# Kernel optimization log

Hardware: AMD Instinct MI355X
Metric: run time of the kernel (lower is better)

The kernel has to match this reference:

```python
import jax, jax.numpy as jnp
import numpy as np

B, N, C, H, D, Kd, Ff, L = 4, 4096, 512, 8, 64, 256, 2048, 2
EPS = 1e-5


def _ln(x, g, b):
    m = x.mean(-1, keepdims=True)
    v = ((x - m) ** 2).mean(-1, keepdims=True)
    return (x - m) / jnp.sqrt(v + EPS) * g + b


def setup_inputs() -> dict:
    key = jax.random.key(0)
    ks = jax.random.split(key, 20)
    s = 0.02
    return {
        'x': jax.random.normal(ks[0], (B, N, C), jnp.float32),
        'Wq': jax.random.normal(ks[1], (L, H, D, C), jnp.float32) * s,
        'Wk': jax.random.normal(ks[2], (L, H, D, C), jnp.float32) * s,
        'Wv': jax.random.normal(ks[3], (L, H, D, C), jnp.float32) * s,
        'Wo': jax.random.normal(ks[4], (L, C, H * D), jnp.float32) * s,
        'bo': jnp.zeros((L, C), jnp.float32),
        'ln1_g': jnp.ones((L, C), jnp.float32),
        'ln1_b': jnp.zeros((L, C), jnp.float32),
        'W1': jax.random.normal(ks[5], (L, Ff, C), jnp.float32) * s,
        'b1': jnp.zeros((L, Ff), jnp.float32),
        'W2': jax.random.normal(ks[6], (L, C, Ff), jnp.float32) * s,
        'b2': jnp.zeros((L, C), jnp.float32),
        'ln2_g': jnp.ones((L, C), jnp.float32),
        'ln2_b': jnp.zeros((L, C), jnp.float32),
        'Ew': jax.random.normal(ks[7], (Kd, N), jnp.float32) * (1.0 / np.sqrt(N)),
        'Eb': jnp.zeros((Kd,), jnp.float32),
    }


def reference(x, Wq, Wk, Wv, Wo, bo, ln1_g, ln1_b, W1, b1, W2, b2, ln2_g, ln2_b, Ew, Eb):
    # Linformer, layerwise-shared E=F projection, causal=False, eval mode (dropout off).
    n_layers = Wq.shape[0]
    d = Wq.shape[2]
    scale = 1.0 / jnp.sqrt(jnp.asarray(d, x.dtype))
    for l in range(n_layers):
        # per-head projections, all heads at once: [b,h,n,d]
        Q = jnp.einsum('bnc,hdc->bhnd', x, Wq[l])
        K = jnp.einsum('bnc,hdc->bhnd', x, Wk[l])
        V = jnp.einsum('bnc,hdc->bhnd', x, Wv[l])
        # E projection along seq axis: K^T [b,h,d,n] -> [b,h,d,k]
        Kp = jnp.einsum('bhnd,kn->bhdk', K, Ew) + Eb[None, None, None, :]
        P = jax.nn.softmax(jnp.einsum('bhnd,bhdk->bhnk', Q, Kp) * scale, axis=-1)
        # F projection (= E, layerwise sharing): V^T -> [b,h,k,d]
        Vp = jnp.einsum('bhnd,kn->bhkd', V, Ew) + Eb[None, None, :, None]
        o = jnp.einsum('bhnk,bhkd->bhnd', P, Vp)
        b_, h_, n_, d_ = o.shape
        o = o.transpose(0, 2, 1, 3).reshape(b_, n_, h_ * d_)  # concat heads
        o = o @ Wo[l].T + bo[l]
        x = _ln(x + o, ln1_g[l], ln1_b[l])  # post-norm residual
        f = jax.nn.gelu(x @ W1[l].T + b1[l], approximate=False) @ W2[l].T + b2[l]
        x = _ln(x + f, ln2_g[l], ln2_b[l])
    return x
```

## Files before the change

kernel.cpp:

```cpp
#include <hip/hip_runtime.h>
#include <math.h>

typedef unsigned short u16;
typedef __attribute__((ext_vector_type(8))) short short8;
typedef __attribute__((ext_vector_type(4))) float f32x4;

#define B_ 4
#define N_ 4096
#define C_ 512
#define H_ 8
#define D_ 64
#define KD_ 256
#define FF_ 2048
#define L_ 2

__device__ __forceinline__ float bf2f(u16 x) {
  return __builtin_bit_cast(float, (unsigned int)x << 16);
}
__device__ __forceinline__ u16 f2bf(float f) {
  unsigned int t = __builtin_bit_cast(unsigned int, f);
  return (u16)((t + 0x7fffu + ((t >> 16) & 1u)) >> 16);
}

#define GLD(g, l)                                                             \
  __builtin_amdgcn_global_load_lds(                                           \
      (const __attribute__((address_space(1))) void*)(g),                     \
      (__attribute__((address_space(3))) void*)(l), 16, 0, 0)

#define MFMA16 __builtin_amdgcn_mfma_f32_16x16x32_bf16

__global__ __launch_bounds__(256) void cvt_kernel(const float* __restrict__ in,
                                                  u16* __restrict__ out, int n4) {
  int i = blockIdx.x * 256 + threadIdx.x;
  if (i >= n4) return;
  float4 v = reinterpret_cast<const float4*>(in)[i];
  ushort4 o;
  o.x = f2bf(v.x); o.y = f2bf(v.y); o.z = f2bf(v.z); o.w = f2bf(v.w);
  reinterpret_cast<ushort4*>(out)[i] = o;
}

__global__ __launch_bounds__(256) void transpose_kernel(const u16* __restrict__ in,
                                                        u16* __restrict__ out) {
  __shared__ u16 T[64][72];
  int n0 = blockIdx.x * 64, c0 = blockIdx.y * 64, b = blockIdx.z;
  const u16* src = in + (long)b * N_ * C_;
  u16* dst = out + (long)b * C_ * N_;
  int t = threadIdx.x;
  int r = t >> 3, cq = (t & 7) * 8;
#pragma unroll
  for (int h = 0; h < 2; ++h) {
    const u16* p = src + (long)(n0 + r + h * 32) * C_ + c0 + cq;
    ushort4 v0 = *reinterpret_cast<const ushort4*>(p);
    ushort4 v1 = *reinterpret_cast<const ushort4*>(p + 4);
    T[r + h * 32][cq + 0] = v0.x; T[r + h * 32][cq + 1] = v0.y;
    T[r + h * 32][cq + 2] = v0.z; T[r + h * 32][cq + 3] = v0.w;
    T[r + h * 32][cq + 4] = v1.x; T[r + h * 32][cq + 5] = v1.y;
    T[r + h * 32][cq + 6] = v1.z; T[r + h * 32][cq + 7] = v1.w;
  }
  __syncthreads();
  int cc = t >> 3, nq = (t & 7) * 8;
#pragma unroll
  for (int h = 0; h < 2; ++h) {
    int cl = cc + h * 32;
    ushort4 w0, w1;
    w0.x = T[nq + 0][cl]; w0.y = T[nq + 1][cl];
    w0.z = T[nq + 2][cl]; w0.w = T[nq + 3][cl];
    w1.x = T[nq + 4][cl]; w1.y = T[nq + 5][cl];
    w1.z = T[nq + 6][cl]; w1.w = T[nq + 7][cl];
    u16* q = dst + (long)(c0 + cl) * N_ + n0 + nq;
    *reinterpret_cast<ushort4*>(q) = w0;
    *reinterpret_cast<ushort4*>(q + 4) = w1;
  }
}

template <int BN, int WM, int WN, int EPI>
__global__ __launch_bounds__(512, 2) void gemm8p(
    const u16* __restrict__ A, const u16* __restrict__ B, u16* __restrict__ C,
    const float* __restrict__ bias, const float* __restrict__ acc32,
    float* __restrict__ out32, int K, int lda, int ldb, int ldc) {
  constexpr int BM = 256, BK = 32;
  constexpr int GB = (BN * BK) / (512 * 8);
  constexpr int G = 2 + GB;
  constexpr int FM = WM / 16, FN = WN / 16;
  constexpr int NWN = BN / WN;
  constexpr int FM0 = FM / 2;

  __shared__ __attribute__((aligned(16))) u16 As[4][BM * BK];
  __shared__ __attribute__((aligned(16))) u16 Bs[4][BN * BK];

  int gy = gridDim.y;
  int nwg = gridDim.x * gy;
  int id = blockIdx.x * gy + blockIdx.y;
  int nid = (id & 7) * (nwg >> 3) + (id >> 3);
  int row0 = (nid / gy) * BM, col0 = (nid % gy) * BN;

  int tid = threadIdx.x;
  int lane = tid & 63, wid = tid >> 6;
  int wr = wid / NWN, wc = wid % NWN;
  int lr = lane & 15, q = lane >> 4;

  auto stA = [&](int buf, int k0) {
#pragma unroll
    for (int g = 0; g < 2; ++g) {
      int c = g * 512 + tid;
      int r = c >> 2, ck = c & 3;
      GLD(A + (long)(row0 + r) * lda + k0 + ((ck ^ ((r >> 1) & 3)) << 3),
          &As[buf][c * 8]);
    }
  };
  auto stB = [&](int buf, int k0) {
#pragma unroll
    for (int g = 0; g < GB; ++g) {
      int c = g * 512 + tid;
      int r = c >> 2, ck = c & 3;
      GLD(B + (long)(col0 + r) * ldb + k0 + ((ck ^ ((r >> 1) & 3)) << 3),
          &Bs[buf][c * 8]);
    }
  };
  auto rd = [&](const u16* Tb, int r) {
    return *reinterpret_cast<const short8*>(&Tb[r * 32 + ((q ^ ((r >> 1) & 3)) << 3)]);
  };

  f32x4 acc[FM][FN] = {};
  int NT = K / BK;

  stA(0, 0); stB(0, 0);
  stA(1, BK); stB(1, BK);
  stA(2, 2 * BK); stB(2, 2 * BK);

  for (int t = 0; t < NT; ++t) {
    const u16* Ab = As[t & 3];
    const u16* Bb = Bs[t & 3];
    bool pf = (t + 3) < NT;
    int bn = (t + 3) & 3, kn = (t + 3) * BK;

    if constexpr (G == 4) asm volatile("s_waitcnt vmcnt(8)" ::: "memory");
    else                  asm volatile("s_waitcnt vmcnt(6)" ::: "memory");
    __builtin_amdgcn_s_barrier();

    short8 bf[FN], af[FM0];
#pragma unroll
    for (int nj = 0; nj < FN; ++nj) bf[nj] = rd(Bb, wc * WN + nj * 16 + lr);
#pragma unroll
    for (int mi = 0; mi < FM0; ++mi) af[mi] = rd(Ab, wr * WM + mi * 16 + lr);
    if (pf) stA(bn, kn);
    __builtin_amdgcn_s_barrier();
    asm volatile("s_waitcnt lgkmcnt(0)" ::: "memory");
    __builtin_amdgcn_sched_barrier(0);
    __builtin_amdgcn_s_setprio(1);
#pragma unroll
    for (int mi = 0; mi < FM0; ++mi)
#pragma unroll
      for (int nj = 0; nj < FN; ++nj)
        acc[mi][nj] = MFMA16(af[mi], bf[nj], acc[mi][nj], 0, 0, 0);
    __builtin_amdgcn_s_setprio(0);
    __builtin_amdgcn_s_barrier();
#pragma unroll
    for (int mi = 0; mi < FM - FM0; ++mi)
      af[mi] = rd(Ab, wr * WM + (FM0 + mi) * 16 + lr);
    if (pf) stB(bn, kn);
    __builtin_amdgcn_s_barrier();
    asm volatile("s_waitcnt lgkmcnt(0)" ::: "memory");
    __builtin_amdgcn_sched_barrier(0);
    __builtin_amdgcn_s_setprio(1);
#pragma unroll
    for (int mi = 0; mi < FM - FM0; ++mi)
#pragma unroll
      for (int nj = 0; nj < FN; ++nj)
        acc[FM0 + mi][nj] = MFMA16(af[mi], bf[nj], acc[FM0 + mi][nj], 0, 0, 0);
    __builtin_amdgcn_s_setprio(0);
    __builtin_amdgcn_s_barrier();
  }

  int lc = lane & 15, rb = (lane >> 4) * 4;
#pragma unroll
  for (int mi = 0; mi < FM; ++mi) {
#pragma unroll
    for (int nj = 0; nj < FN; ++nj) {
      int j = col0 + wc * WN + nj * 16 + lc;
      int m0 = row0 + wr * WM + mi * 16 + rb;
#pragma unroll
      for (int r = 0; r < 4; ++r) {
        long m = m0 + r;
        float v = acc[mi][nj][r];
        if constexpr (EPI == 0) {
          C[m * ldc + j] = f2bf(v);
        } else if constexpr (EPI == 1) {
          C[m * ldc + j] = f2bf(v + bias[j]);
        } else if constexpr (EPI == 2) {
          float tt = v + bias[j];
          float u = tt * (0.7978845608f + 0.0356774081f * tt * tt);
          float e = __expf(2.f * u);
          float th = 1.f - 2.f / (e + 1.f);
          C[m * ldc + j] = f2bf(0.5f * tt * (1.f + th));
        } else if constexpr (EPI == 8) {
          out32[m * ldc + j] = v;
        } else {
          C[m * ldc + j] = f2bf(v + acc32[m * ldc + j] + bias[j]);
        }
      }
    }
  }
}

template <int BM, int BN, int EPI, int SPLITK>
__global__ __launch_bounds__(256, 2) void gemm_nt(
    const u16* __restrict__ A, const u16* __restrict__ B, void* __restrict__ Cout,
    const float* __restrict__ bias, int K, int lda, int ldb, int ldc,
    long sA0, long sA1, long sB0, long sB1, long sC0, long sC1, long sCh,
    int nz, float alpha) {
  constexpr int BK = 64;
  constexpr int WM = BM / 2, WN = BN / 2;
  constexpr int FM = WM / 16, FN = WN / 16;
  constexpr int CA = BM / 32, CB = BN / 32;

  __shared__ __attribute__((aligned(16))) u16 As[BM * BK];
  __shared__ __attribute__((aligned(16))) u16 Bs[BN * BK];

  int z, chunk;
  if constexpr (SPLITK > 1) { z = blockIdx.z % nz; chunk = blockIdx.z / nz; }
  else { z = blockIdx.z; chunk = 0; }
  int zb = z >> 3, zh = z & 7;
  A += (long)zb * sA0 + (long)zh * sA1;
  B += (long)zb * sB0 + (long)zh * sB1;
  long coff = (long)zb * sC0 + (long)zh * sC1 + (long)chunk * sCh;

  int tid = threadIdx.x;
  int lane = tid & 63, wid = tid >> 6;
  int wr = wid >> 1, wc = wid & 1;
  int row0 = blockIdx.x * BM, col0 = blockIdx.y * BN;

  int Kc = K / SPLITK;
  int kbeg = chunk * Kc;

  f32x4 acc[FM][FN] = {};

  for (int k0 = kbeg; k0 < kbeg + Kc; k0 += BK) {
#pragma unroll
    for (int i = 0; i < CA; ++i) {
      int c = tid + i * 256;
      GLD(A + (long)(row0 + (c >> 3)) * lda + k0 + (c & 7) * 8, As + c * 8);
    }
#pragma unroll
    for (int i = 0; i < CB; ++i) {
      int c = tid + i * 256;
      GLD(B + (long)(col0 + (c >> 3)) * ldb + k0 + (c & 7) * 8, Bs + c * 8);
    }
    __syncthreads();

    int lr = lane & 15, lk = (lane >> 4) * 8;
#pragma unroll
    for (int kk = 0; kk < BK; kk += 32) {
      short8 af[FM], bfr[FN];
#pragma unroll
      for (int mi = 0; mi < FM; ++mi)
        af[mi] = *reinterpret_cast<const short8*>(&As[(wr * WM + mi * 16 + lr) * BK + kk + lk]);
#pragma unroll
      for (int nj = 0; nj < FN; ++nj)
        bfr[nj] = *reinterpret_cast<const short8*>(&Bs[(wc * WN + nj * 16 + lr) * BK + kk + lk]);
#pragma unroll
      for (int mi = 0; mi < FM; ++mi)
#pragma unroll
        for (int nj = 0; nj < FN; ++nj)
          acc[mi][nj] = MFMA16(af[mi], bfr[nj], acc[mi][nj], 0, 0, 0);
    }
    __syncthreads();
  }

  int lc = lane & 15, rb = (lane >> 4) * 4;
#pragma unroll
  for (int mi = 0; mi < FM; ++mi) {
#pragma unroll
    for (int nj = 0; nj < FN; ++nj) {
      int j = col0 + wc * WN + nj * 16 + lc;
      int m0 = row0 + wr * WM + mi * 16 + rb;
#pragma unroll
      for (int r = 0; r < 4; ++r) {
        int m = m0 + r;
        float v = acc[mi][nj][r];
        if constexpr (EPI == 4) {
          reinterpret_cast<u16*>(Cout)[coff + (long)m * ldc + j] = f2bf(v + bias[m]);
        } else if constexpr (EPI == 6) {
          reinterpret_cast<u16*>(Cout)[coff + (long)j * ldc + m] = f2bf(v + bias[m]);
        } else {
          reinterpret_cast<float*>(Cout)[coff + (long)m * ldc + j] = v;
        }
      }
    }
  }
}

__global__ __launch_bounds__(256) void reduce8_kernel(const float* __restrict__ part,
                                                      u16* __restrict__ out) {
  int i = blockIdx.x * 256 + threadIdx.x;
  const float4* p = reinterpret_cast<const float4*>(part);
  float4 s = p[i];
#pragma unroll
  for (int c = 1; c < 8; ++c) {
    float4 t = p[i + c * 131072];
    s.x += t.x; s.y += t.y; s.z += t.z; s.w += t.w;
  }
  ushort4 o;
  o.x = f2bf(s.x); o.y = f2bf(s.y); o.z = f2bf(s.z); o.w = f2bf(s.w);
  reinterpret_cast<ushort4*>(out)[i] = o;
}

__global__ __launch_bounds__(512, 2) void attn_kernel(
    const u16* __restrict__ Q, const u16* __restrict__ Kp,
    const u16* __restrict__ Vpt, u16* __restrict__ O) {
  constexpr int LQ = 72, LKP = 72, LVP = 264, LP = 264;
  __shared__ __attribute__((aligned(16))) u16 Q_s[128 * LQ];
  __shared__ __attribute__((aligned(16))) u16 Kp_s[256 * LKP];
  __shared__ __attribute__((aligned(16))) u16 Vp_s[64 * LVP];
  __shared__ __attribute__((aligned(16))) u16 P_s[128 * LP];

  int n0 = blockIdx.x * 128;
  int bh = blockIdx.y;
  int b = bh >> 3, h = bh & 7;
  long qbase = ((long)b * N_ + n0) * 512 + h * 64;
  const u16* Kpb = Kp + ((long)b * KD_) * 512 + h * 64;
  const u16* Vpb = Vpt + ((long)b * 512 + h * 64) * KD_;

  int tid = threadIdx.x;
#pragma unroll
  for (int i = 0; i < 2; ++i) {
    int c = tid + i * 512;
    int r = c >> 3, c8 = (c & 7) * 8;
    *reinterpret_cast<uint4*>(&Q_s[r * LQ + c8]) =
        *reinterpret_cast<const uint4*>(Q + qbase + (long)r * 512 + c8);
  }
#pragma unroll
  for (int i = 0; i < 4; ++i) {
    int c = tid + i * 512;
    int r = c >> 3, c8 = (c & 7) * 8;
    *reinterpret_cast<uint4*>(&Kp_s[r * LKP + c8]) =
        *reinterpret_cast<const uint4*>(Kpb + (long)r * 512 + c8);
  }
#pragma unroll
  for (int i = 0; i < 4; ++i) {
    int c = tid + i * 512;
    int r = c >> 5, c8 = (c & 31) * 8;
    *reinterpret_cast<uint4*>(&Vp_s[r * LVP + c8]) =
        *reinterpret_cast<const uint4*>(Vpb + (long)r * KD_ + c8);
  }
  __syncthreads();

  int lane = tid & 63, w = tid >> 6;
  int q0 = w * 16;
  int lr = lane & 15, lk = (lane >> 4) * 8;
  int lc = lane & 15, rb = (lane >> 4) * 4;

  f32x4 acc[16] = {};
  short8 af0 = *reinterpret_cast<const short8*>(&Q_s[(q0 + lr) * LQ + lk]);
  short8 af1 = *reinterpret_cast<const short8*>(&Q_s[(q0 + lr) * LQ + 32 + lk]);
#pragma unroll
  for (int t = 0; t < 16; ++t) {
    short8 b0 = *reinterpret_cast<const short8*>(&Kp_s[(t * 16 + lr) * LKP + lk]);
    short8 b1 = *reinterpret_cast<const short8*>(&Kp_s[(t * 16 + lr) * LKP + 32 + lk]);
    acc[t] = MFMA16(af0, b0, acc[t], 0, 0, 0);
    acc[t] = MFMA16(af1, b1, acc[t], 0, 0, 0);
  }

  float mx[4] = {-3.4e38f, -3.4e38f, -3.4e38f, -3.4e38f};
#pragma unroll
  for (int t = 0; t < 16; ++t)
#pragma unroll
    for (int r = 0; r < 4; ++r) {
      acc[t][r] *= 0.125f;
      mx[r] = fmaxf(mx[r], acc[t][r]);
    }
#pragma unroll
  for (int o = 1; o < 16; o <<= 1)
#pragma unroll
    for (int r = 0; r < 4; ++r) mx[r] = fmaxf(mx[r], __shfl_xor(mx[r], o));
  float sm[4] = {0.f, 0.f, 0.f, 0.f};
#pragma unroll
  for (int t = 0; t < 16; ++t)
#pragma unroll
    for (int r = 0; r < 4; ++r) {
      float e = __expf(acc[t][r] - mx[r]);
      acc[t][r] = e;
      sm[r] += e;
    }
#pragma unroll
  for (int o = 1; o < 16; o <<= 1)
#pragma unroll
    for (int r = 0; r < 4; ++r) sm[r] += __shfl_xor(sm[r], o);
  float inv[4];
#pragma unroll
  for (int r = 0; r < 4; ++r) inv[r] = 1.f / sm[r];
#pragma unroll
  for (int t = 0; t < 16; ++t)
#pragma unroll
    for (int r = 0; r < 4; ++r)
      P_s[(q0 + rb + r) * LP + t * 16 + lc] = f2bf(acc[t][r] * inv[r]);

  f32x4 o2[4] = {};
#pragma unroll
  for (int kk = 0; kk < 8; ++kk) {
    short8 pa = *reinterpret_cast<const short8*>(&P_s[(q0 + lr) * LP + kk * 32 + lk]);
#pragma unroll
    for (int nj = 0; nj < 4; ++nj) {
      short8 vb = *reinterpret_cast<const short8*>(&Vp_s[(nj * 16 + lr) * LVP + kk * 32 + lk]);
      o2[nj] = MFMA16(pa, vb, o2[nj], 0, 0, 0);
    }
  }
#pragma unroll
  for (int nj = 0; nj < 4; ++nj)
#pragma unroll
    for (int r = 0; r < 4; ++r)
      O[qbase + (long)(q0 + rb + r) * 512 + nj * 16 + lc] = f2bf(o2[nj][r]);
}

__global__ __launch_bounds__(256) void add_ln_kernel(
    const float* __restrict__ xin32, const u16* __restrict__ xinb,
    const u16* __restrict__ yin, const float* __restrict__ g,
    const float* __restrict__ bt, float* __restrict__ xout32,
    u16* __restrict__ xbout) {
  int row = blockIdx.x * 4 + (threadIdx.x >> 6);
  int lane = threadIdx.x & 63;
  long base = (long)row * C_ + lane * 8;
  float s[8];
  if (xin32) {
    float4 a0 = *reinterpret_cast<const float4*>(xin32 + base);
    float4 a1 = *reinterpret_cast<const float4*>(xin32 + base + 4);
    s[0] = a0.x; s[1] = a0.y; s[2] = a0.z; s[3] = a0.w;
    s[4] = a1.x; s[5] = a1.y; s[6] = a1.z; s[7] = a1.w;
  } else {
    ushort4 x0 = *reinterpret_cast<const ushort4*>(xinb + base);
    ushort4 x1 = *reinterpret_cast<const ushort4*>(xinb + base + 4);
    s[0] = bf2f(x0.x); s[1] = bf2f(x0.y); s[2] = bf2f(x0.z); s[3] = bf2f(x0.w);
    s[4] = bf2f(x1.x); s[5] = bf2f(x1.y); s[6] = bf2f(x1.z); s[7] = bf2f(x1.w);
  }
  ushort4 u0 = *reinterpret_cast<const ushort4*>(yin + base);
  ushort4 u1 = *reinterpret_cast<const ushort4*>(yin + base + 4);
  s[0] += bf2f(u0.x); s[1] += bf2f(u0.y); s[2] += bf2f(u0.z); s[3] += bf2f(u0.w);
  s[4] += bf2f(u1.x); s[5] += bf2f(u1.y); s[6] += bf2f(u1.z); s[7] += bf2f(u1.w);
  float sum = 0.f;
#pragma unroll
  for (int i = 0; i < 8; ++i) sum += s[i];
#pragma unroll
  for (int o = 1; o < 64; o <<= 1) sum += __shfl_xor(sum, o);
  float mean = sum * (1.f / C_);
  float var = 0.f;
#pragma unroll
  for (int i = 0; i < 8; ++i) { float d = s[i] - mean; var += d * d; }
#pragma unroll
  for (int o = 1; o < 64; o <<= 1) var += __shfl_xor(var, o);
  float inv = rsqrtf(var * (1.f / C_) + 1e-5f);
  int c0 = lane * 8;
  float o[8];
#pragma unroll
  for (int i = 0; i < 8; ++i) o[i] = (s[i] - mean) * inv * g[c0 + i] + bt[c0 + i];
  if (xout32) {
    float4 f0 = {o[0], o[1], o[2], o[3]};
    float4 f1 = {o[4], o[5], o[6], o[7]};
    *reinterpret_cast<float4*>(xout32 + base) = f0;
    *reinterpret_cast<float4*>(xout32 + base + 4) = f1;
  }
  if (xbout) {
    ushort4 w0 = {f2bf(o[0]), f2bf(o[1]), f2bf(o[2]), f2bf(o[3])};
    ushort4 w1 = {f2bf(o[4]), f2bf(o[5]), f2bf(o[6]), f2bf(o[7])};
    *reinterpret_cast<ushort4*>(xbout + base) = w0;
    *reinterpret_cast<ushort4*>(xbout + base + 4) = w1;
  }
}

extern "C" void kernel_launch(void* const* d_in, const int* in_sizes, int n_in,
                              void* d_out, int out_size, void* d_ws, size_t ws_size,
                              hipStream_t stream) {
  const float* x    = (const float*)d_in[0];
  const float* Wq   = (const float*)d_in[1];
  const float* Wk   = (const float*)d_in[2];
  const float* Wv   = (const float*)d_in[3];
  const float* Wo   = (const float*)d_in[4];
  const float* bo   = (const float*)d_in[5];
  const float* ln1g = (const float*)d_in[6];
  const float* ln1b = (const float*)d_in[7];
  const float* W1   = (const float*)d_in[8];
  const float* b1   = (const float*)d_in[9];
  const float* W2   = (const float*)d_in[10];
  const float* b2   = (const float*)d_in[11];
  const float* ln2g = (const float*)d_in[12];
  const float* ln2b = (const float*)d_in[13];
  const float* Ew   = (const float*)d_in[14];
  const float* Eb   = (const float*)d_in[15];
  float* xc = (float*)d_out;

  char* wsp = (char*)d_ws;
  size_t off = 0;
  auto alloc = [&](size_t bytes) -> void* {
    void* p = wsp + off;
    off = (off + bytes + 255) & ~(size_t)255;
    return p;
  };
  u16* xb  = (u16*)alloc(8388608UL * 2);
  u16* BIG = (u16*)alloc(16777216UL * 2);
  u16* Qb  = (u16*)alloc(8388608UL * 2);
  u16* yb  = (u16*)alloc(8388608UL * 2);
  u16* xEb = (u16*)alloc(524288UL * 2);
  u16* Kpb = (u16*)alloc(524288UL * 2);
  u16* Vpt = (u16*)alloc(524288UL * 2);
  u16* wqb = (u16*)alloc(524288UL * 2);
  u16* wkb = (u16*)alloc(524288UL * 2);
  u16* wvb = (u16*)alloc(524288UL * 2);
  u16* wob = (u16*)alloc(524288UL * 2);
  u16* w1b = (u16*)alloc(2097152UL * 2);
  u16* w2b = (u16*)alloc(2097152UL * 2);
  u16* ewb = (u16*)alloc(1048576UL * 2);
  (void)ws_size; (void)in_sizes; (void)n_in; (void)out_size;

  auto cvt = [&](const float* src, u16* dst, long n) {
    int n4 = (int)(n / 4);
    cvt_kernel<<<dim3((n4 + 255) / 256), dim3(256), 0, stream>>>(src, dst, n4);
  };
  cvt(x, xb, 8388608);
  cvt(Wq, wqb, 524288);
  cvt(Wk, wkb, 524288);
  cvt(Wv, wvb, 524288);
  cvt(Wo, wob, 524288);
  cvt(W1, w1b, 2097152);
  cvt(W2, w2b, 2097152);
  cvt(Ew, ewb, 1048576);

  for (int l = 0; l < L_; ++l) {
    const u16* wq = wqb + (long)l * 262144;
    const u16* wk = wkb + (long)l * 262144;
    const u16* wv = wvb + (long)l * 262144;
    const u16* wo = wob + (long)l * 262144;
    const u16* w1 = w1b + (long)l * 1048576;
    const u16* w2 = w2b + (long)l * 1048576;

    u16* xT = BIG;
    float* partF = (float*)(BIG + 8388608);
    transpose_kernel<<<dim3(64, 8, 4), dim3(256), 0, stream>>>(xb, xT);
    gemm_nt<128, 128, 7, 8><<<dim3(2, 4, 32), dim3(256), 0, stream>>>(
        ewb, xT, partF, nullptr, 4096, 4096, 4096, 512,
        0, 0, 0, 2097152, 0, 131072, 524288, 4, 1.f);
    reduce8_kernel<<<dim3(512), dim3(256), 0, stream>>>(partF, xEb);
    gemm_nt<128, 128, 4, 1><<<dim3(2, 4, 4), dim3(256), 0, stream>>>(
        xEb, wk, Kpb, Eb, 512, 512, 512, 512,
        0, 131072, 0, 0, 0, 131072, 0, 4, 1.f);
    gemm_nt<128, 128, 6, 1><<<dim3(2, 4, 4), dim3(256), 0, stream>>>(
        xEb, wv, Vpt, Eb, 512, 512, 512, 256,
        0, 131072, 0, 0, 0, 131072, 0, 4, 1.f);
    gemm8p<128, 64, 64, 0><<<dim3(64, 4), dim3(512), 0, stream>>>(
        xb, wq, Qb, nullptr, nullptr, nullptr, 512, 512, 512, 512);

    attn_kernel<<<dim3(32, 32), dim3(512), 0, stream>>>(Qb, Kpb, Vpt, Qb);

    gemm8p<128, 64, 64, 1><<<dim3(64, 4), dim3(512), 0, stream>>>(
        Qb, wo, yb, bo + (long)l * 512, nullptr, nullptr, 512, 512, 512, 512);
    add_ln_kernel<<<dim3(4096), dim3(256), 0, stream>>>(
        l == 0 ? x : nullptr, l == 0 ? nullptr : xb, yb,
        ln1g + (long)l * 512, ln1b + (long)l * 512, nullptr, xb);

    for (int ch = 0; ch < 2; ++ch) {
      u16* h1 = BIG;
      gemm8p<256, 128, 64, 2><<<dim3(64, 4), dim3(512), 0, stream>>>(
          xb, w1 + (long)ch * 1024 * 512, h1, b1 + (long)l * 2048 + ch * 1024,
          nullptr, nullptr, 512, 512, 512, 1024);
      if (ch == 0) {
        gemm8p<128, 64, 64, 8><<<dim3(64, 4), dim3(512), 0, stream>>>(
            h1, w2 + 0, nullptr, nullptr, nullptr, xc, 1024, 1024, 2048, 512);
      } else {
        gemm8p<128, 64, 64, 9><<<dim3(64, 4), dim3(512), 0, stream>>>(
            h1, w2 + 1024, yb, b2 + (long)l * 512, xc, nullptr, 1024, 1024, 2048, 512);
      }
    }
    add_ln_kernel<<<dim3(4096), dim3(256), 0, stream>>>(
        nullptr, xb, yb, ln2g + (long)l * 512, ln2b + (long)l * 512,
        (l == L_ - 1) ? xc : nullptr, (l == L_ - 1) ? (u16*)nullptr : xb);
  }
}
```

Measured before the change: 588.2 us.

## Restructure FFN into full-width GEMMs with split-K bf16 partials folded into LayerNorm

```diff
diff --git a/kernel.cpp b/kernel.cpp
--- a/kernel.cpp
+++ b/kernel.cpp
@@ -37,6 +37,24 @@
   ushort4 o;
   o.x = f2bf(v.x); o.y = f2bf(v.y); o.z = f2bf(v.z); o.w = f2bf(v.w);
   reinterpret_cast<ushort4*>(out)[i] = o;
+}
+
+struct Segs {
+  const float* src[7];
+  u16* dst[7];
+  int endblk[7];
+};
+__global__ __launch_bounds__(256) void cvt_multi_kernel(Segs sg) {
+  int b = blockIdx.x;
+  int i = 0;
+#pragma unroll
+  for (int k = 0; k < 6; ++k) i += (b >= sg.endblk[k]);
+  int start = (i == 0) ? 0 : sg.endblk[i - 1];
+  int idx = (b - start) * 256 + threadIdx.x;
+  float4 v = reinterpret_cast<const float4*>(sg.src[i])[idx];
+  ushort4 o;
+  o.x = f2bf(v.x); o.y = f2bf(v.y); o.z = f2bf(v.z); o.w = f2bf(v.w);
+  reinterpret_cast<ushort4*>(sg.dst[i])[idx] = o;
 }
 
 __global__ __launch_bounds__(256) void transpose_kernel(const u16* __restrict__ in,
@@ -73,20 +91,22 @@
   }
 }
 
-template <int BN, int WM, int WN, int EPI>
+template <int BM, int BN, int WM, int WN, int EPI>
 __global__ __launch_bounds__(512, 2) void gemm8p(
     const u16* __restrict__ A, const u16* __restrict__ B, u16* __restrict__ C,
-    const float* __restrict__ bias, const float* __restrict__ acc32,
-    float* __restrict__ out32, int K, int lda, int ldb, int ldc) {
-  constexpr int BM = 256, BK = 32;
-  constexpr int GB = (BN * BK) / (512 * 8);
-  constexpr int G = 2 + GB;
-  constexpr int FM = WM / 16, FN = WN / 16;
+    const float* __restrict__ bias, int K, int lda, int ldb, int ldc,
+    long sAz, long sBz, long sCz) {
+  constexpr int BK = 32;
+  constexpr int GA = BM / 128, GB = BN / 128, G = GA + GB;
+  constexpr int FM = WM / 16, FN = WN / 16, FM0 = FM / 2;
   constexpr int NWN = BN / WN;
-  constexpr int FM0 = FM / 2;
 
   __shared__ __attribute__((aligned(16))) u16 As[4][BM * BK];
   __shared__ __attribute__((aligned(16))) u16 Bs[4][BN * BK];
+
+  A += (long)blockIdx.z * sAz;
+  B += (long)blockIdx.z * sBz;
+  C += (long)blockIdx.z * sCz;
 
   int gy = gridDim.y;
   int nwg = gridDim.x * gy;
@@ -101,7 +121,7 @@
 
   auto stA = [&](int buf, int k0) {
 #pragma unroll
-    for (int g = 0; g < 2; ++g) {
+    for (int g = 0; g < GA; ++g) {
       int c = g * 512 + tid;
       int r = c >> 2, ck = c & 3;
       GLD(A + (long)(row0 + r) * lda + k0 + ((ck ^ ((r >> 1) & 3)) << 3),
@@ -187,16 +207,12 @@
           C[m * ldc + j] = f2bf(v);
         } else if constexpr (EPI == 1) {
           C[m * ldc + j] = f2bf(v + bias[j]);
-        } else if constexpr (EPI == 2) {
+        } else {
           float tt = v + bias[j];
           float u = tt * (0.7978845608f + 0.0356774081f * tt * tt);
           float e = __expf(2.f * u);
           float th = 1.f - 2.f / (e + 1.f);
           C[m * ldc + j] = f2bf(0.5f * tt * (1.f + th));
-        } else if constexpr (EPI == 8) {
-          out32[m * ldc + j] = v;
-        } else {
-          C[m * ldc + j] = f2bf(v + acc32[m * ldc + j] + bias[j]);
         }
       }
     }
@@ -205,10 +221,10 @@
 
 template <int BM, int BN, int EPI, int SPLITK>
 __global__ __launch_bounds__(256, 2) void gemm_nt(
-    const u16* __restrict__ A, const u16* __restrict__ B, void* __restrict__ Cout,
+    const u16* __restrict__ A, const u16* B, void* __restrict__ Cout,
     const float* __restrict__ bias, int K, int lda, int ldb, int ldc,
-    long sA0, long sA1, long sB0, long sB1, long sC0, long sC1, long sCh,
-    int nz, float alpha) {
+    long sA1, long sB1, long sC1, long sCh, int nz, float alpha,
+    const u16* __restrict__ B2, void* __restrict__ Cout2) {
   constexpr int BK = 64;
   constexpr int WM = BM / 2, WN = BN / 2;
   constexpr int FM = WM / 16, FN = WN / 16;
@@ -217,13 +233,23 @@
   __shared__ __attribute__((aligned(16))) u16 As[BM * BK];
   __shared__ __attribute__((aligned(16))) u16 Bs[BN * BK];
 
-  int z, chunk;
-  if constexpr (SPLITK > 1) { z = blockIdx.z % nz; chunk = blockIdx.z / nz; }
-  else { z = blockIdx.z; chunk = 0; }
-  int zb = z >> 3, zh = z & 7;
-  A += (long)zb * sA0 + (long)zh * sA1;
-  B += (long)zb * sB0 + (long)zh * sB1;
-  long coff = (long)zb * sC0 + (long)zh * sC1 + (long)chunk * sCh;
+  int z, chunk, kv = 0;
+  long coff;
+  if constexpr (EPI == 10) {
+    z = blockIdx.z; chunk = 0;
+    kv = z >> 2;
+    int zbq = z & 3;
+    A += (long)zbq * 131072;
+    if (kv) B = B2;
+    coff = (long)zbq * 131072;
+  } else {
+    if constexpr (SPLITK > 1) { z = blockIdx.z % nz; chunk = blockIdx.z / nz; }
+    else { z = blockIdx.z; chunk = 0; }
+    A += (long)z * 0;
+    A += (long)z * sA1;
+    B += (long)z * sB1;
+    coff = (long)z * sC1 + (long)chunk * sCh;
+  }
 
   int tid = threadIdx.x;
   int lane = tid & 63, wid = tid >> 6;
@@ -278,10 +304,11 @@
       for (int r = 0; r < 4; ++r) {
         int m = m0 + r;
         float v = acc[mi][nj][r];
-        if constexpr (EPI == 4) {
-          reinterpret_cast<u16*>(Cout)[coff + (long)m * ldc + j] = f2bf(v + bias[m]);
-        } else if constexpr (EPI == 6) {
-          reinterpret_cast<u16*>(Cout)[coff + (long)j * ldc + m] = f2bf(v + bias[m]);
+        if constexpr (EPI == 10) {
+          if (kv == 0)
+            reinterpret_cast<u16*>(Cout)[coff + (long)m * 512 + j] = f2bf(v + bias[m]);
+          else
+            reinterpret_cast<u16*>(Cout2)[coff + (long)j * 256 + m] = f2bf(v + bias[m]);
         } else {
           reinterpret_cast<float*>(Cout)[coff + (long)m * ldc + j] = v;
         }
@@ -414,12 +441,14 @@
 
 __global__ __launch_bounds__(256) void add_ln_kernel(
     const float* __restrict__ xin32, const u16* __restrict__ xinb,
-    const u16* __restrict__ yin, const float* __restrict__ g,
+    const u16* __restrict__ yin, const u16* __restrict__ yin2,
+    const float* __restrict__ bias2, const float* __restrict__ g,
     const float* __restrict__ bt, float* __restrict__ xout32,
     u16* __restrict__ xbout) {
   int row = blockIdx.x * 4 + (threadIdx.x >> 6);
   int lane = threadIdx.x & 63;
-  long base = (long)row * C_ + lane * 8;
+  int c0 = lane * 8;
+  long base = (long)row * C_ + c0;
   float s[8];
   if (xin32) {
     float4 a0 = *reinterpret_cast<const float4*>(xin32 + base);
@@ -436,6 +465,16 @@
   ushort4 u1 = *reinterpret_cast<const ushort4*>(yin + base + 4);
   s[0] += bf2f(u0.x); s[1] += bf2f(u0.y); s[2] += bf2f(u0.z); s[3] += bf2f(u0.w);
   s[4] += bf2f(u1.x); s[5] += bf2f(u1.y); s[6] += bf2f(u1.z); s[7] += bf2f(u1.w);
+  if (yin2) {
+    ushort4 v0 = *reinterpret_cast<const ushort4*>(yin2 + base);
+    ushort4 v1 = *reinterpret_cast<const ushort4*>(yin2 + base + 4);
+    s[0] += bf2f(v0.x); s[1] += bf2f(v0.y); s[2] += bf2f(v0.z); s[3] += bf2f(v0.w);
+    s[4] += bf2f(v1.x); s[5] += bf2f(v1.y); s[6] += bf2f(v1.z); s[7] += bf2f(v1.w);
+  }
+  if (bias2) {
+#pragma unroll
+    for (int i = 0; i < 8; ++i) s[i] += bias2[c0 + i];
+  }
   float sum = 0.f;
 #pragma unroll
   for (int i = 0; i < 8; ++i) sum += s[i];
@@ -448,7 +487,6 @@
 #pragma unroll
   for (int o = 1; o < 64; o <<= 1) var += __shfl_xor(var, o);
   float inv = rsqrtf(var * (1.f / C_) + 1e-5f);
-  int c0 = lane * 8;
   float o[8];
 #pragma unroll
   for (int i = 0; i < 8; ++i) o[i] = (s[i] - mean) * inv * g[c0 + i] + bt[c0 + i];
@@ -495,9 +533,10 @@
     return p;
   };
   u16* xb  = (u16*)alloc(8388608UL * 2);
-  u16* BIG = (u16*)alloc(16777216UL * 2);
+  u16* BIG = (u16*)alloc(33554432UL * 2);
   u16* Qb  = (u16*)alloc(8388608UL * 2);
   u16* yb  = (u16*)alloc(8388608UL * 2);
+  u16* Pp  = (u16*)alloc(16777216UL * 2);
   u16* xEb = (u16*)alloc(524288UL * 2);
   u16* Kpb = (u16*)alloc(524288UL * 2);
   u16* Vpt = (u16*)alloc(524288UL * 2);
@@ -510,18 +549,19 @@
   u16* ewb = (u16*)alloc(1048576UL * 2);
   (void)ws_size; (void)in_sizes; (void)n_in; (void)out_size;
 
-  auto cvt = [&](const float* src, u16* dst, long n) {
-    int n4 = (int)(n / 4);
-    cvt_kernel<<<dim3((n4 + 255) / 256), dim3(256), 0, stream>>>(src, dst, n4);
-  };
-  cvt(x, xb, 8388608);
-  cvt(Wq, wqb, 524288);
-  cvt(Wk, wkb, 524288);
-  cvt(Wv, wvb, 524288);
-  cvt(Wo, wob, 524288);
-  cvt(W1, w1b, 2097152);
-  cvt(W2, w2b, 2097152);
-  cvt(Ew, ewb, 1048576);
+  cvt_kernel<<<dim3(8192), dim3(256), 0, stream>>>(x, xb, 2097152);
+  Segs sg;
+  sg.src[0] = Wq; sg.dst[0] = wqb;
+  sg.src[1] = Wk; sg.dst[1] = wkb;
+  sg.src[2] = Wv; sg.dst[2] = wvb;
+  sg.src[3] = Wo; sg.dst[3] = wob;
+  sg.src[4] = W1; sg.dst[4] = w1b;
+  sg.src[5] = W2; sg.dst[5] = w2b;
+  sg.src[6] = Ew; sg.dst[6] = ewb;
+  sg.endblk[0] = 512;  sg.endblk[1] = 1024; sg.endblk[2] = 1536;
+  sg.endblk[3] = 2048; sg.endblk[4] = 4096; sg.endblk[5] = 6144;
+  sg.endblk[6] = 7168;
+  cvt_multi_kernel<<<dim3(7168), dim3(256), 0, stream>>>(sg);
 
   for (int l = 0; l < L_; ++l) {
     const u16* wq = wqb + (long)l * 262144;
@@ -536,40 +576,30 @@
     transpose_kernel<<<dim3(64, 8, 4), dim3(256), 0, stream>>>(xb, xT);
     gemm_nt<128, 128, 7, 8><<<dim3(2, 4, 32), dim3(256), 0, stream>>>(
         ewb, xT, partF, nullptr, 4096, 4096, 4096, 512,
-        0, 0, 0, 2097152, 0, 131072, 524288, 4, 1.f);
+        0, 2097152, 131072, 524288, 4, 1.f, nullptr, nullptr);
     reduce8_kernel<<<dim3(512), dim3(256), 0, stream>>>(partF, xEb);
-    gemm_nt<128, 128, 4, 1><<<dim3(2, 4, 4), dim3(256), 0, stream>>>(
+    gemm_nt<128, 128, 10, 1><<<dim3(2, 4, 8), dim3(256), 0, stream>>>(
         xEb, wk, Kpb, Eb, 512, 512, 512, 512,
-        0, 131072, 0, 0, 0, 131072, 0, 4, 1.f);
-    gemm_nt<128, 128, 6, 1><<<dim3(2, 4, 4), dim3(256), 0, stream>>>(
-        xEb, wv, Vpt, Eb, 512, 512, 512, 256,
-        0, 131072, 0, 0, 0, 131072, 0, 4, 1.f);
-    gemm8p<128, 64, 64, 0><<<dim3(64, 4), dim3(512), 0, stream>>>(
-        xb, wq, Qb, nullptr, nullptr, nullptr, 512, 512, 512, 512);
+        0, 0, 0, 0, 8, 1.f, wv, Vpt);
+    gemm8p<128, 256, 64, 64, 0><<<dim3(128, 2), dim3(512), 0, stream>>>(
+        xb, wq, Qb, nullptr, 512, 512, 512, 512, 0, 0, 0);
 
     attn_kernel<<<dim3(32, 32), dim3(512), 0, stream>>>(Qb, Kpb, Vpt, Qb);
 
-    gemm8p<128, 64, 64, 1><<<dim3(64, 4), dim3(512), 0, stream>>>(
-        Qb, wo, yb, bo + (long)l * 512, nullptr, nullptr, 512, 512, 512, 512);
+    gemm8p<128, 256, 64, 64, 1><<<dim3(128, 2), dim3(512), 0, stream>>>(
+        Qb, wo, yb, bo + (long)l * 512, 512, 512, 512, 512, 0, 0, 0);
     add_ln_kernel<<<dim3(4096), dim3(256), 0, stream>>>(
-        l == 0 ? x : nullptr, l == 0 ? nullptr : xb, yb,
+        l == 0 ? x : nullptr, l == 0 ? nullptr : xb, yb, nullptr, nullptr,
         ln1g + (long)l * 512, ln1b + (long)l * 512, nullptr, xb);
 
-    for (int ch = 0; ch < 2; ++ch) {
-      u16* h1 = BIG;
-      gemm8p<256, 128, 64, 2><<<dim3(64, 4), dim3(512), 0, stream>>>(
-          xb, w1 + (long)ch * 1024 * 512, h1, b1 + (long)l * 2048 + ch * 1024,
-          nullptr, nullptr, 512, 512, 512, 1024);
-      if (ch == 0) {
-        gemm8p<128, 64, 64, 8><<<dim3(64, 4), dim3(512), 0, stream>>>(
-            h1, w2 + 0, nullptr, nullptr, nullptr, xc, 1024, 1024, 2048, 512);
-      } else {
-        gemm8p<128, 64, 64, 9><<<dim3(64, 4), dim3(512), 0, stream>>>(
-            h1, w2 + 1024, yb, b2 + (long)l * 512, xc, nullptr, 1024, 1024, 2048, 512);
-      }
-    }
+    u16* h1 = BIG;
+    gemm8p<256, 256, 128, 64, 2><<<dim3(64, 8), dim3(512), 0, stream>>>(
+        xb, w1, h1, b1 + (long)l * 2048, 512, 512, 512, 2048, 0, 0, 0);
+    gemm8p<256, 256, 128, 64, 0><<<dim3(64, 2, 2), dim3(512), 0, stream>>>(
+        h1, w2, Pp, nullptr, 1024, 2048, 2048, 512, 1024, 1024, 8388608);
     add_ln_kernel<<<dim3(4096), dim3(256), 0, stream>>>(
-        nullptr, xb, yb, ln2g + (long)l * 512, ln2b + (long)l * 512,
+        nullptr, xb, Pp, Pp + 8388608, b2 + (long)l * 512,
+        ln2g + (long)l * 512, ln2b + (long)l * 512,
         (l == L_ - 1) ? xc : nullptr, (l == L_ - 1) ? (u16*)nullptr : xb);
   }
 }
```

Measured after the change: 586.1 us. Within noise of the previous version (-0.3%).
